# Optimization experiments

Hardware: AMD Instinct MI355X
Metric: run time of the kernel (lower is better)

## Reference

```python
import jax, jax.numpy as jnp
import numpy as np

B = 65536   # batch
F = 256     # FeatureDim
E = 8       # experts_num
D = 64      # ExpertOutDim
EPS = 1e-5  # BatchNorm eps (eval mode: running stats)


def _bn(x, g, be, m, v):
    # BatchNorm1d in eval mode
    return (x - m) * jax.lax.rsqrt(v + EPS) * g + be


def setup_inputs() -> dict:
    key = jax.random.key(0)
    ks = jax.random.split(key, 40)
    r = lambda i, s: jax.random.normal(ks[i], s, dtype=jnp.float32) * 0.05
    u = lambda i, s: jax.random.uniform(ks[i], s, dtype=jnp.float32)
    return dict(
        signal_em=jax.random.normal(ks[0], (B, F), dtype=jnp.float32),
        muti_em=jax.random.normal(ks[1], (B, F), dtype=jnp.float32),
        similarity=jax.random.uniform(ks[2], (B,), dtype=jnp.float32),
        w=u(3, ()), b=u(4, ()),
        ps_W=r(5, (F, 256)), ps_b=r(6, (256,)), ps_g=u(7, (256,)), ps_be=r(8, (256,)), ps_m=r(9, (256,)), ps_v=u(10, (256,)) + 0.5,
        pm_W=r(11, (F, 256)), pm_b=r(12, (256,)), pm_g=u(13, (256,)), pm_be=r(14, (256,)), pm_m=r(15, (256,)), pm_v=u(16, (256,)) + 0.5,
        c1_W=r(17, (2 * F, 64)), c1_b=r(18, (64,)), c1_g=u(19, (64,)), c1_be=r(20, (64,)), c1_m=r(21, (64,)), c1_v=u(22, (64,)) + 0.5,
        c2_W=r(23, (64, 64)), c2_b=r(24, (64,)), c2_g=u(25, (64,)), c2_be=r(26, (64,)), c2_m=r(27, (64,)), c2_v=u(28, (64,)) + 0.5,
        c3_W=r(29, (64, 2)), c3_b=r(30, (2,)),
        e_W1=r(31, (E, 2 * F, 256)), e_b1=r(32, (E, 256)),
        e_W2=r(33, (E, 256, D)), e_b2=r(34, (E, D)),
        s_W1=r(35, (E, E)), s_b1=r(36, (E,)), s_W2=r(37, (E, E)), s_b2=r(38, (E,)),
    )


def reference(signal_em, muti_em, similarity, w, b,
              ps_W, ps_b, ps_g, ps_be, ps_m, ps_v,
              pm_W, pm_b, pm_g, pm_be, pm_m, pm_v,
              c1_W, c1_b, c1_g, c1_be, c1_m, c1_v,
              c2_W, c2_b, c2_g, c2_be, c2_m, c2_v,
              c3_W, c3_b,
              e_W1, e_b1, e_W2, e_b2,
              s_W1, s_b1, s_W2, s_b2):
    sim_weight = similarity[:, None] * w + b                        # [B,1]
    sig = jax.nn.relu(_bn(signal_em @ ps_W + ps_b, ps_g, ps_be, ps_m, ps_v))
    sig = sim_weight * sig
    mut = jax.nn.relu(_bn(muti_em @ pm_W + pm_b, pm_g, pm_be, pm_m, pm_v))
    temp = jnp.concatenate([sig, mut], axis=1)                      # [B, 512]

    # classifier head (dropout = identity in eval mode)
    h = jax.nn.relu(_bn(temp @ c1_W + c1_b, c1_g, c1_be, c1_m, c1_v))
    h = jax.nn.relu(_bn(h @ c2_W + c2_b, c2_g, c2_be, c2_m, c2_v))
    pre_score = h @ c3_W + c3_b                                     # [B,2]

    # all E experts as one batched GEMM (Expert_net has dropout p=0)
    eh = jax.nn.relu(jnp.einsum('bf,efh->beh', temp, e_W1) + e_b1)  # [B,E,256]
    eo = jax.nn.relu(jnp.einsum('beh,ehd->bed', eh, e_W2) + e_b2)   # [B,E,64]

    # SE-style gating: avg/max pool over expert-out dim (kernel==D -> scalar)
    att_ave = eo.mean(axis=-1)                                      # [B,E]
    att_max = eo.max(axis=-1)                                       # [B,E]
    senet = lambda x: jax.nn.gelu(x @ s_W1 + s_b1, approximate=False) @ s_W2 + s_b2
    wts = jax.nn.sigmoid(senet(att_ave) + senet(att_max))           # [B,E]

    gate_out = jnp.einsum('bed,be->bd', eo, wts)                    # [B,D]
    return (gate_out, pre_score)
```

## Files before the change

kernel.cpp:

```cpp
#include <hip/hip_runtime.h>
#include <math.h>

using u32 = unsigned int;
using u16 = unsigned short;
typedef __attribute__((ext_vector_type(4))) float f4;
typedef __attribute__((ext_vector_type(4))) u32 u4;
typedef __attribute__((ext_vector_type(2))) u32 u2;
typedef __attribute__((ext_vector_type(8))) __bf16 b8;

union U4B8 { u4 u; b8 b; };

__device__ __forceinline__ u16 f2b(float x) {
  u32 u = __float_as_uint(x);
  u32 r = (u + 0x7FFFu + ((u >> 16) & 1u)) >> 16;
  return (u16)r;
}
__device__ __forceinline__ u32 pack2(float a, float b) { return (u32)f2b(a) | ((u32)f2b(b) << 16); }
__device__ __forceinline__ f4 mfma16(b8 a, b8 b, f4 c) {
  return __builtin_amdgcn_mfma_f32_16x16x32_bf16(a, b, c, 0, 0, 0);
}

#define FENCE() asm volatile("" ::: "memory")
#define RAWBAR() do { FENCE(); __builtin_amdgcn_s_barrier(); FENCE(); __builtin_amdgcn_sched_barrier(0); } while (0)
#define VMW(nlit) do { asm volatile("s_waitcnt vmcnt(" nlit ")" ::: "memory"); __builtin_amdgcn_sched_barrier(0); } while (0)
#define LGKM0() do { asm volatile("s_waitcnt lgkmcnt(0)" ::: "memory"); __builtin_amdgcn_sched_barrier(0); } while (0)
#define LBAR() do { LGKM0(); __builtin_amdgcn_s_barrier(); FENCE(); __builtin_amdgcn_sched_barrier(0); } while (0)

template <int NB>
__device__ __forceinline__ void gstage(const u16* g, u16* l, int t) {
#pragma unroll
  for (int i = 0; i < NB; i += 8192) {
    __builtin_amdgcn_global_load_lds(
        (__attribute__((address_space(1))) u32*)(g + (i >> 1) + t * 8),
        (__attribute__((address_space(3))) u32*)(l + (i >> 1) + ((t >> 6) << 9)),
        16, 0, 0);
  }
}

__global__ void prep_kernel(
    const float* __restrict__ ps_W, const float* __restrict__ ps_b, const float* __restrict__ ps_g,
    const float* __restrict__ ps_be, const float* __restrict__ ps_m, const float* __restrict__ ps_v,
    const float* __restrict__ pm_W, const float* __restrict__ pm_b, const float* __restrict__ pm_g,
    const float* __restrict__ pm_be, const float* __restrict__ pm_m, const float* __restrict__ pm_v,
    const float* __restrict__ c1_W, const float* __restrict__ c1_b, const float* __restrict__ c1_g,
    const float* __restrict__ c1_be, const float* __restrict__ c1_m, const float* __restrict__ c1_v,
    const float* __restrict__ c2_W, const float* __restrict__ c2_b, const float* __restrict__ c2_g,
    const float* __restrict__ c2_be, const float* __restrict__ c2_m, const float* __restrict__ c2_v,
    u16* __restrict__ pst, u16* __restrict__ pmt,
    u16* __restrict__ c1t, u16* __restrict__ c2t, float* __restrict__ fold)
{
  int i0 = blockIdx.x * blockDim.x + threadIdx.x;
  int stride = gridDim.x * blockDim.x;
  for (int idx = i0; idx < 65536; idx += stride) {
    int s = idx >> 14; int rem = idx & 16383;
    int n = rem >> 6, q = rem & 63;
    int k = s * 64 + (q ^ ((n & 7) << 3));
    pst[idx] = f2b(ps_W[k * 256 + n]);
    pmt[idx] = f2b(pm_W[k * 256 + n]);
  }
  for (int idx = i0; idx < 64 * 512; idx += stride) {
    int n = idx >> 9, q = idx & 511;
    int k = q ^ ((n & 7) << 3);
    c1t[idx] = f2b(c1_W[k * 64 + n]);
  }
  for (int idx = i0; idx < 64 * 64; idx += stride) {
    int n = idx >> 6, k = idx & 63;
    c2t[idx] = f2b(c2_W[k * 64 + n]);
  }
  for (int idx = i0; idx < 256; idx += stride) {
    float a = ps_g[idx] * rsqrtf(ps_v[idx] + 1e-5f);
    fold[idx] = a; fold[256 + idx] = (ps_b[idx] - ps_m[idx]) * a + ps_be[idx];
    float a2 = pm_g[idx] * rsqrtf(pm_v[idx] + 1e-5f);
    fold[512 + idx] = a2; fold[768 + idx] = (pm_b[idx] - pm_m[idx]) * a2 + pm_be[idx];
  }
  for (int idx = i0; idx < 64; idx += stride) {
    float a = c1_g[idx] * rsqrtf(c1_v[idx] + 1e-5f);
    fold[1024 + idx] = a; fold[1088 + idx] = (c1_b[idx] - c1_m[idx]) * a + c1_be[idx];
    float a2 = c2_g[idx] * rsqrtf(c2_v[idx] + 1e-5f);
    fold[1152 + idx] = a2; fold[1216 + idx] = (c2_b[idx] - c2_m[idx]) * a2 + c2_be[idx];
  }
}

__global__ __launch_bounds__(512, 4) void k1_kernel(
    const float* __restrict__ sig, const float* __restrict__ mut,
    const float* __restrict__ simil, const float* __restrict__ wS, const float* __restrict__ bS,
    const u16* __restrict__ pst, const u16* __restrict__ pmt,
    const float* __restrict__ fold, u16* __restrict__ temp,
    const float* __restrict__ e_W1, const float* __restrict__ e_W2,
    u16* __restrict__ w1t, u16* __restrict__ w2t)
{
  extern __shared__ __align__(16) u16 smk[];
  const int t = threadIdx.x;
  if (blockIdx.y == 2) {
    int i0 = blockIdx.x * 512 + t;
    const int stride = 1024 * 512;
    for (int idx = i0; idx < 8 * 256 * 512; idx += stride) {
      int e = idx >> 17; int rem = idx & 131071;
      int s = rem >> 14; int rem2 = rem & 16383;
      int n = rem2 >> 6; int q = rem2 & 63;
      int k = s * 64 + (q ^ ((n & 7) << 3));
      w1t[idx] = f2b(e_W1[e * 131072 + k * 256 + n]);
    }
    for (int idx = i0; idx < 8 * 64 * 256; idx += stride) {
      int e = idx >> 14; int rem = idx & 16383;
      int d = rem >> 8; int q = rem & 255;
      int h = q ^ ((d & 7) << 3);
      w2t[idx] = f2b(e_W2[e * 16384 + h * 64 + d]);
    }
    return;
  }
  const int w = t >> 6, l = t & 63;
  const int lr = l & 15, lk = (l >> 4) * 8, lv = (l >> 4) * 4;
  const int xoru = (l & 7) << 3;
  const int rg = w >> 1, cg = w & 1;
  const int half = blockIdx.y;
  const float* X = half ? mut : sig;
  const u16* Wt = half ? pmt : pst;
  const int rb = blockIdx.x;
  const int rg0 = rb * 64;
  const f4 ZF = {0.f, 0.f, 0.f, 0.f};
  const int myrow = rg * 16 + lr;

  f4 xr[16];
  {
    const float* xp = X + (rg0 + myrow) * 256 + lk;
#pragma unroll
    for (int c = 0; c < 8; ++c) {
      xr[2 * c]     = *(const f4*)(xp + c * 32);
      xr[2 * c + 1] = *(const f4*)(xp + c * 32 + 4);
    }
  }
  float swv = 1.f;
  if (half == 0) swv = simil[rg0 + myrow] * wS[0] + bS[0];
  gstage<32768>(Wt, smk, t);
  b8 af[8];
#pragma unroll
  for (int c = 0; c < 8; ++c) {
    U4B8 tmp;
    tmp.u[0] = pack2(xr[2 * c][0], xr[2 * c][1]);
    tmp.u[1] = pack2(xr[2 * c][2], xr[2 * c][3]);
    tmp.u[2] = pack2(xr[2 * c + 1][0], xr[2 * c + 1][1]);
    tmp.u[3] = pack2(xr[2 * c + 1][2], xr[2 * c + 1][3]);
    af[c] = tmp.b;
  }

  f4 acc[8];
#pragma unroll
  for (int i = 0; i < 8; ++i) acc[i] = ZF;

#define K1P(P, STG) do { \
    VMW("0"); RAWBAR(); \
    STG; \
    __builtin_amdgcn_s_setprio(1); \
    _Pragma("unroll") for (int kk = 0; kk < 2; ++kk) { \
      b8 bf[8]; \
      _Pragma("unroll") for (int nf = 0; nf < 8; ++nf) \
        bf[nf] = *(const b8*)(smk + ((P) & 1) * 16384 + (cg * 128 + nf * 16 + lr) * 64 + ((kk * 32 + lk) ^ xoru)); \
      _Pragma("unroll") for (int nf = 0; nf < 8; ++nf) \
        acc[nf] = mfma16(bf[nf], af[(P) * 2 + kk], acc[nf]); \
    } \
    __builtin_amdgcn_s_setprio(0); \
  } while (0)

  K1P(0, gstage<32768>(Wt + 16384, smk + 16384, t));
  K1P(1, gstage<32768>(Wt + 32768, smk, t));
  K1P(2, gstage<32768>(Wt + 49152, smk + 16384, t));
  K1P(3, (void)0);
#undef K1P

#pragma unroll
  for (int nf = 0; nf < 8; ++nf) {
    int col = cg * 128 + nf * 16 + lv;
    const f4 al = *(const f4*)(fold + half * 512 + col);
    const f4 be = *(const f4*)(fold + half * 512 + 256 + col);
    float v0 = fmaxf(acc[nf][0] * al[0] + be[0], 0.f) * swv;
    float v1 = fmaxf(acc[nf][1] * al[1] + be[1], 0.f) * swv;
    float v2 = fmaxf(acc[nf][2] * al[2] + be[2], 0.f) * swv;
    float v3 = fmaxf(acc[nf][3] * al[3] + be[3], 0.f) * swv;
    u2 pv; pv[0] = pack2(v0, v1); pv[1] = pack2(v2, v3);
    int st = col >> 6;
    int kin = col & 63;
    int q = kin ^ ((myrow & 7) << 3);
    *(u2*)(smk + st * 4096 + myrow * 64 + q) = pv;
  }
  LBAR();
  {
    u16* dst = temp + (rb >> 1) * 65536 + half * 32768 + (rb & 1) * 4096;
#pragma unroll
    for (int st = 0; st < 4; ++st) {
      u4 v = *(const u4*)(smk + st * 4096 + t * 8);
      *(u4*)(dst + st * 8192 + t * 8) = v;
    }
  }
}

__global__ __launch_bounds__(512, 2) void k2_kernel(
    u16* __restrict__ temp, const u16* __restrict__ w1t, const u16* __restrict__ w2t,
    const u16* __restrict__ c1t, const u16* __restrict__ c2t,
    const float* __restrict__ fold,
    const float* __restrict__ c3W, const float* __restrict__ c3B,
    const float* __restrict__ eb1, const float* __restrict__ eb2,
    const float* __restrict__ sW1, const float* __restrict__ sB1,
    const float* __restrict__ sW2, const float* __restrict__ sB2,
    float* __restrict__ outp)
{
  extern __shared__ __align__(16) u16 sm[];
  u16* smW  = sm;
  u16* smE  = sm + 32768;
  u16* smR2 = sm + 49152;
  float* attA  = (float*)(sm + 65536);
  float* attM  = attA + 1024;
  float* wtsb  = attM + 1024;
  float* c3sm  = wtsb + 1024;
  float* eb1sm = c3sm + 136;
  float* eb2sm = eb1sm + 2048;

  const int t = threadIdx.x, w = t >> 6, l = t & 63;
  const int lr = l & 15, lk = (l >> 4) * 8, lv = (l >> 4) * 4;
  const int xoru = (l & 7) << 3;
  const int rg = w >> 1, cg = w & 1;
  const int rg0 = blockIdx.x * 128;
  const f4 ZF = {0.f, 0.f, 0.f, 0.f};
  u16* tempE = temp + blockIdx.x * 65536;

  b8 af[16][2];

#define AFLOAD(R) { \
    _Pragma("unroll") for (int c8 = 0; c8 < 8; ++c8) { \
      _Pragma("unroll") for (int mi = 0; mi < 2; ++mi) \
        af[(R) * 8 + c8][mi] = *(const b8*)(smE + (c8 >> 1) * 8192 + (rg * 32 + mi * 16 + lr) * 64 + ((((c8 & 1) * 32) + lk) ^ xoru)); \
    } }

  {
    for (int z = t; z < 2048; z += 512) attA[z] = 0.f;
    f4 rEb1 = *(const f4*)(eb1 + t * 4);
    f4 rEb2 = ZF; if (t < 128) rEb2 = *(const f4*)(eb2 + t * 4);
    float rC3 = 0.f; if (t < 128) rC3 = c3W[t]; else if (t < 130) rC3 = c3B[t - 128];
    u4 rC2 = *(const u4*)(c2t + (t >> 3) * 64 + (t & 7) * 8);

    gstage<65536>(tempE, smE, t);
    gstage<65536>(c1t, smW, t);
    *(f4*)(eb1sm + t * 4) = rEb1;
    if (t < 128) *(f4*)(eb2sm + t * 4) = rEb2;
    if (t < 130) c3sm[t] = rC3;
    VMW("8"); RAWBAR();
    AFLOAD(0);
    asm volatile("s_waitcnt lgkmcnt(0)" ::: "memory");
    RAWBAR();
    gstage<65536>(tempE + 32768, smE, t);
    VMW("8"); RAWBAR();
    f4 ah[2][2] = {{ZF, ZF}, {ZF, ZF}};
#define HPART(R) { \
    __builtin_amdgcn_s_setprio(1); \
    _Pragma("unroll") for (int c8 = 0; c8 < 8; ++c8) { \
      _Pragma("unroll") for (int nf = 0; nf < 2; ++nf) { \
        b8 ch = *(const b8*)(smW + (cg * 32 + nf * 16 + lr) * 512 + ((((R) * 8 + c8) * 32 + lk) ^ xoru)); \
        _Pragma("unroll") for (int mi = 0; mi < 2; ++mi) \
          ah[nf][mi] = mfma16(ch, af[(R) * 8 + c8][mi], ah[nf][mi]); \
      } } \
    __builtin_amdgcn_s_setprio(0); }
    HPART(0)
    VMW("0"); RAWBAR();
    AFLOAD(1);
    HPART(1)
#undef HPART
    asm volatile("s_waitcnt lgkmcnt(0)" ::: "memory");
    RAWBAR();
    u16* h1b = smE;
    u16* c2sm = smR2;
    u16* h2b = smR2 + 4608;
#pragma unroll
    for (int nf = 0; nf < 2; ++nf) {
      int col = cg * 32 + nf * 16 + lv;
      const f4 av1 = *(const f4*)(fold + 1024 + col);
      const f4 bv1 = *(const f4*)(fold + 1088 + col);
#pragma unroll
      for (int mi = 0; mi < 2; ++mi) {
        int row = rg * 32 + mi * 16 + lr;
        u2 pv;
        pv[0] = pack2(fmaxf(ah[nf][mi][0] * av1[0] + bv1[0], 0.f), fmaxf(ah[nf][mi][1] * av1[1] + bv1[1], 0.f));
        pv[1] = pack2(fmaxf(ah[nf][mi][2] * av1[2] + bv1[2], 0.f), fmaxf(ah[nf][mi][3] * av1[3] + bv1[3], 0.f));
        *(u2*)(h1b + row * 72 + col) = pv;
      }
    }
    *(u4*)(c2sm + (t >> 3) * 72 + (t & 7) * 8) = rC2;
    LBAR();
    f4 a2[2][2] = {{ZF, ZF}, {ZF, ZF}};
#pragma unroll
    for (int kk = 0; kk < 2; ++kk) {
      b8 hf[2], cf[2];
#pragma unroll
      for (int mi = 0; mi < 2; ++mi)
        hf[mi] = *(const b8*)(h1b + (rg * 32 + mi * 16 + lr) * 72 + kk * 32 + lk);
#pragma unroll
      for (int nf = 0; nf < 2; ++nf)
        cf[nf] = *(const b8*)(c2sm + (cg * 32 + nf * 16 + lr) * 72 + kk * 32 + lk);
#pragma unroll
      for (int mi = 0; mi < 2; ++mi)
#pragma unroll
        for (int nf = 0; nf < 2; ++nf)
          a2[mi][nf] = mfma16(cf[nf], hf[mi], a2[mi][nf]);
    }
#pragma unroll
    for (int nf = 0; nf < 2; ++nf) {
      int col = cg * 32 + nf * 16 + lv;
      const f4 av2 = *(const f4*)(fold + 1152 + col);
      const f4 bv2 = *(const f4*)(fold + 1216 + col);
#pragma unroll
      for (int mi = 0; mi < 2; ++mi) {
        int row = rg * 32 + mi * 16 + lr;
        u2 pv;
        pv[0] = pack2(fmaxf(a2[mi][nf][0] * av2[0] + bv2[0], 0.f), fmaxf(a2[mi][nf][1] * av2[1] + bv2[1], 0.f));
        pv[1] = pack2(fmaxf(a2[mi][nf][2] * av2[2] + bv2[2], 0.f), fmaxf(a2[mi][nf][3] * av2[3] + bv2[3], 0.f));
        *(u2*)(h2b + row * 72 + col) = pv;
      }
    }
    LBAR();
    if (t < 256) {
      int row = t >> 1, c = t & 1;
      float s_ = c3sm[128 + c];
#pragma unroll
      for (int j = 0; j < 8; ++j) {
        u4 hv = *(const u4*)(h2b + row * 72 + j * 8);
#pragma unroll
        for (int q = 0; q < 4; ++q) {
          float lo = __uint_as_float(hv[q] << 16);
          float hi = __uint_as_float(hv[q] & 0xffff0000u);
          s_ += lo * c3sm[(j * 8 + q * 2) * 2 + c];
          s_ += hi * c3sm[(j * 8 + q * 2 + 1) * 2 + c];
        }
      }
      outp[4194304 + (rg0 + row) * 2 + c] = s_;
    }
    RAWBAR();
    gstage<32768>(w1t, smW, t);
  }

#define MPH(P, NW, ...) do { \
    VMW(NW); RAWBAR(); \
    __VA_ARGS__; \
    __builtin_amdgcn_s_setprio(1); \
    _Pragma("unroll") for (int kk = 0; kk < 2; ++kk) { \
      b8 bfA[4], bfB[4]; \
      _Pragma("unroll") for (int nf = 0; nf < 4; ++nf) \
        bfA[nf] = *(const b8*)(smW + ((P) & 1) * 16384 + (cg * 64 + nf * 16 + lr) * 64 + ((kk * 32 + lk) ^ xoru)); \
      _Pragma("unroll") for (int nf = 0; nf < 4; ++nf) \
        bfB[nf] = *(const b8*)(smW + ((P) & 1) * 16384 + 8192 + (cg * 64 + nf * 16 + lr) * 64 + ((kk * 32 + lk) ^ xoru)); \
      _Pragma("unroll") for (int nf = 0; nf < 4; ++nf) \
        _Pragma("unroll") for (int mi = 0; mi < 2; ++mi) \
          acc[nf][mi] = mfma16(bfA[nf], af[(P) * 2 + kk][mi], acc[nf][mi]); \
      _Pragma("unroll") for (int nf = 0; nf < 4; ++nf) \
        _Pragma("unroll") for (int mi = 0; mi < 2; ++mi) \
          acc[4 + nf][mi] = mfma16(bfB[nf], af[(P) * 2 + kk][mi], acc[4 + nf][mi]); \
    } \
    __builtin_amdgcn_s_setprio(0); \
  } while (0)

#define EHEPI(E, H, DST) { \
    _Pragma("unroll") for (int nf = 0; nf < 4; ++nf) { \
      int colL = cg * 64 + nf * 16 + lv; \
      const f4 bv = *(const f4*)(eb1sm + (E) * 256 + (H) * 128 + colL); \
      _Pragma("unroll") for (int mi = 0; mi < 2; ++mi) { \
        int row = rg * 32 + mi * 16 + lr; \
        f4 a_ = acc[(H) * 4 + nf][mi]; \
        u2 pv; \
        pv[0] = pack2(fmaxf(a_[0] + bv[0], 0.f), fmaxf(a_[1] + bv[1], 0.f)); \
        pv[1] = pack2(fmaxf(a_[2] + bv[2], 0.f), fmaxf(a_[3] + bv[3], 0.f)); \
        *(u2*)((DST) + row * 128 + (colL ^ xoru)) = pv; \
      } } }

#define G2ALL() do { \
    __builtin_amdgcn_s_setprio(1); \
    _Pragma("unroll") for (int kq = 0; kq < 8; ++kq) { \
      const u16* ebase = (kq < 4) ? smE : (smW + 16384); \
      b8 wf[2], ef[2]; \
      _Pragma("unroll") for (int nf = 0; nf < 2; ++nf) \
        wf[nf] = *(const b8*)(smR2 + (cg * 32 + nf * 16 + lr) * 256 + ((kq * 32 + lk) ^ xoru)); \
      _Pragma("unroll") for (int mi = 0; mi < 2; ++mi) \
        ef[mi] = *(const b8*)(ebase + (rg * 32 + mi * 16 + lr) * 128 + ((((kq & 3) * 32) + lk) ^ xoru)); \
      _Pragma("unroll") for (int mi = 0; mi < 2; ++mi) \
        _Pragma("unroll") for (int nf = 0; nf < 2; ++nf) \
          e2[mi][nf] = mfma16(wf[nf], ef[mi], e2[mi][nf]); \
    } \
    __builtin_amdgcn_s_setprio(0); \
  } while (0)

#define EXPERT(E, NWP0, NWG2) { \
    const u16* w1E = w1t + (E) * 131072; \
    f4 acc[8][2]; \
    _Pragma("unroll") for (int nf = 0; nf < 8; ++nf) \
      _Pragma("unroll") for (int mi = 0; mi < 2; ++mi) acc[nf][mi] = ZF; \
    MPH(0, NWP0, gstage<32768>(w1E + 1 * 16384, smW + 16384, t)); \
    MPH(1, "0",  gstage<32768>(w1E + 2 * 16384, smW, t)); \
    MPH(2, "0",  gstage<32768>(w1E + 3 * 16384, smW + 16384, t)); \
    MPH(3, "0",  gstage<32768>(w1E + 4 * 16384, smW, t)); \
    MPH(4, "0",  gstage<32768>(w1E + 5 * 16384, smW + 16384, t)); \
    MPH(5, "0",  gstage<32768>(w1E + 6 * 16384, smW, t)); \
    MPH(6, "0",  { gstage<32768>(w1E + 7 * 16384, smW + 16384, t); \
                   gstage<32768>(w2t + (E) * 16384, smR2, t); }); \
    MPH(7, "4",  { if ((E) < 7) gstage<32768>(w1t + ((E) + 1) * 131072, smW, t); }); \
    EHEPI(E, 0, smE) \
    RAWBAR();  \
    EHEPI(E, 1, smW + 16384) \
    VMW(NWG2); LBAR();  \
    f4 e2[2][2]; \
    e2[0][0] = ZF; e2[0][1] = ZF; e2[1][0] = ZF; e2[1][1] = ZF; \
    G2ALL(); \
     \
    _Pragma("unroll") for (int mi = 0; mi < 2; ++mi) { \
      int row = rg * 32 + mi * 16 + lr; \
      float s_ = 0.f, mx = 0.f; \
      _Pragma("unroll") for (int nf = 0; nf < 2; ++nf) { \
        int d0 = cg * 32 + nf * 16 + lv; \
        const f4 bv2 = *(const f4*)(eb2sm + (E) * 64 + d0); \
        float v0 = fmaxf(e2[mi][nf][0] + bv2[0], 0.f); \
        float v1 = fmaxf(e2[mi][nf][1] + bv2[1], 0.f); \
        float v2 = fmaxf(e2[mi][nf][2] + bv2[2], 0.f); \
        float v3 = fmaxf(e2[mi][nf][3] + bv2[3], 0.f); \
        s_ += v0 + v1 + v2 + v3; \
        mx = fmaxf(mx, fmaxf(fmaxf(v0, v1), fmaxf(v2, v3))); \
        u2 pv; pv[0] = pack2(v0, v1); pv[1] = pack2(v2, v3); \
        *(u2*)(tempE + (E) * 8192 + row * 64 + d0) = pv; \
      } \
      s_ += __shfl_xor(s_, 16); s_ += __shfl_xor(s_, 32); \
      mx = fmaxf(mx, __shfl_xor(mx, 16)); mx = fmaxf(mx, __shfl_xor(mx, 32)); \
      if (l < 16) { \
        atomicAdd(attA + row * 8 + (E), s_); \
        atomicMax((unsigned int*)(attM + row * 8 + (E)), __float_as_uint(mx)); \
      } \
    } \
  }

  EXPERT(0, "0", "4")
  EXPERT(1, "4", "4")
  EXPERT(2, "4", "4")
  EXPERT(3, "4", "4")
  EXPERT(4, "4", "4")
  EXPERT(5, "4", "4")
  EXPERT(6, "4", "4")
  EXPERT(7, "4", "0")
#undef EXPERT
#undef MPH
#undef EHEPI
#undef G2ALL

  VMW("0");
  LBAR();
  if (t < 128) {
    float xa[8], xm[8], ga[8], gm[8];
#pragma unroll
    for (int j = 0; j < 8; ++j) {
      xa[j] = attA[t * 8 + j] * 0.015625f;
      xm[j] = attM[t * 8 + j];
    }
#pragma unroll
    for (int j = 0; j < 8; ++j) {
      float a1 = sB1[j], a2 = sB1[j];
#pragma unroll
      for (int i = 0; i < 8; ++i) { float wv = sW1[i * 8 + j]; a1 += xa[i] * wv; a2 += xm[i] * wv; }
      ga[j] = 0.5f * a1 * (1.f + erff(a1 * 0.70710678118654752f));
      gm[j] = 0.5f * a2 * (1.f + erff(a2 * 0.70710678118654752f));
    }
#pragma unroll
    for (int j = 0; j < 8; ++j) {
      float o1 = sB2[j], o2 = sB2[j];
#pragma unroll
      for (int i = 0; i < 8; ++i) { float wv = sW2[i * 8 + j]; o1 += ga[i] * wv; o2 += gm[i] * wv; }
      float z = o1 + o2;
      wtsb[t * 8 + j] = 1.f / (1.f + expf(-z));
    }
  }
  LBAR();
  {
    int grow = t >> 2, gd0 = (t & 3) * 16;
    float wv[8];
#pragma unroll
    for (int e2_ = 0; e2_ < 8; ++e2_) wv[e2_] = wtsb[grow * 8 + e2_];
    float g[16];
#pragma unroll
    for (int j = 0; j < 16; ++j) g[j] = 0.f;
#pragma unroll
    for (int e2_ = 0; e2_ < 8; ++e2_) {
      const u16* wsE = tempE + e2_ * 8192 + grow * 64 + gd0;
      u4 qa = *(const u4*)(wsE); u4 qb = *(const u4*)(wsE + 8);
#pragma unroll
      for (int q = 0; q < 4; ++q) {
        g[2 * q + 0] += wv[e2_] * __uint_as_float(qa[q] << 16);
        g[2 * q + 1] += wv[e2_] * __uint_as_float(qa[q] & 0xffff0000u);
        g[8 + 2 * q + 0] += wv[e2_] * __uint_as_float(qb[q] << 16);
        g[8 + 2 * q + 1] += wv[e2_] * __uint_as_float(qb[q] & 0xffff0000u);
      }
    }
    float* op = outp + (rg0 + grow) * 64 + gd0;
    f4 o0 = {g[0], g[1], g[2], g[3]}, o1 = {g[4], g[5], g[6], g[7]};
    f4 o2 = {g[8], g[9], g[10], g[11]}, o3 = {g[12], g[13], g[14], g[15]};
    *(f4*)op = o0; *(f4*)(op + 4) = o1; *(f4*)(op + 8) = o2; *(f4*)(op + 12) = o3;
  }
}

extern "C" void kernel_launch(void* const* d_in, const int* in_sizes, int n_in,
                              void* d_out, int out_size, void* d_ws, size_t ws_size,
                              hipStream_t stream) {
  const float* signal = (const float*)d_in[0];
  const float* muti   = (const float*)d_in[1];
  const float* simil  = (const float*)d_in[2];
  const float* wS     = (const float*)d_in[3];
  const float* bS     = (const float*)d_in[4];
  const float* ps_W = (const float*)d_in[5];  const float* ps_b = (const float*)d_in[6];
  const float* ps_g = (const float*)d_in[7];  const float* ps_be = (const float*)d_in[8];
  const float* ps_m = (const float*)d_in[9];  const float* ps_v = (const float*)d_in[10];
  const float* pm_W = (const float*)d_in[11]; const float* pm_b = (const float*)d_in[12];
  const float* pm_g = (const float*)d_in[13]; const float* pm_be = (const float*)d_in[14];
  const float* pm_m = (const float*)d_in[15]; const float* pm_v = (const float*)d_in[16];
  const float* c1_W = (const float*)d_in[17]; const float* c1_b = (const float*)d_in[18];
  const float* c1_g = (const float*)d_in[19]; const float* c1_be = (const float*)d_in[20];
  const float* c1_m = (const float*)d_in[21]; const float* c1_v = (const float*)d_in[22];
  const float* c2_W = (const float*)d_in[23]; const float* c2_b = (const float*)d_in[24];
  const float* c2_g = (const float*)d_in[25]; const float* c2_be = (const float*)d_in[26];
  const float* c2_m = (const float*)d_in[27]; const float* c2_v = (const float*)d_in[28];
  const float* c3_W = (const float*)d_in[29]; const float* c3_b = (const float*)d_in[30];
  const float* e_W1 = (const float*)d_in[31]; const float* e_b1 = (const float*)d_in[32];
  const float* e_W2 = (const float*)d_in[33]; const float* e_b2 = (const float*)d_in[34];
  const float* s_W1 = (const float*)d_in[35]; const float* s_b1 = (const float*)d_in[36];
  const float* s_W2 = (const float*)d_in[37]; const float* s_b2 = (const float*)d_in[38];

  char* ws = (char*)d_ws;
  u16* temp = (u16*)ws;
  u16* w1t  = (u16*)(ws + 67108864);
  u16* w2t  = (u16*)(ws + 69206016);
  u16* pst  = (u16*)(ws + 69468160);
  u16* pmt  = (u16*)(ws + 69599232);
  u16* c1t  = (u16*)(ws + 69730304);
  u16* c2t  = (u16*)(ws + 69795840);
  float* fold = (float*)(ws + 69804032);
  float* outp = (float*)d_out;

  prep_kernel<<<dim3(256), dim3(256), 0, stream>>>(
      ps_W, ps_b, ps_g, ps_be, ps_m, ps_v, pm_W, pm_b, pm_g, pm_be, pm_m, pm_v,
      c1_W, c1_b, c1_g, c1_be, c1_m, c1_v, c2_W, c2_b, c2_g, c2_be, c2_m, c2_v,
      pst, pmt, c1t, c2t, fold);
  k1_kernel<<<dim3(1024, 3), dim3(512), 65536, stream>>>(
      signal, muti, simil, wS, bS, pst, pmt, fold, temp, e_W1, e_W2, w1t, w2t);
  k2_kernel<<<dim3(512), dim3(512), 154144, stream>>>(
      temp, w1t, w2t, c1t, c2t, fold, c3_W, c3_b, e_b1, e_b2, s_W1, s_b1, s_W2, s_b2, outp);
}
```

Before: 261.7 us.

## Load half of expert W1 fragments directly from global into registers

Splits each expert's first-layer weights into two halves. Columns 0-127 are still staged through shared memory. Columns 128-255 are pre-laid out in MFMA fragment order so each lane can load them straight from global memory into registers. This halves the LDS staging buffer for W1, which frees shared memory so the expert hidden upper half (ehHi) gets its own region and one barrier goes away. The c1 weight layout changes to match. In exchange the kernel issues more global loads per wave, carries more registers, and depends on finer vmcnt wait tuning.

```diff
diff --git a/kernel.cpp b/kernel.cpp
--- a/kernel.cpp
+++ b/kernel.cpp
@@ -59,8 +59,9 @@
     pmt[idx] = f2b(pm_W[k * 256 + n]);
   }
   for (int idx = i0; idx < 64 * 512; idx += stride) {
-    int n = idx >> 9, q = idx & 511;
-    int k = q ^ ((n & 7) << 3);
+    int R = idx >> 14; int rem = idx & 16383;
+    int n = rem >> 8, q = rem & 255;
+    int k = R * 256 + (q ^ ((n & 7) << 3));
     c1t[idx] = f2b(c1_W[k * 64 + n]);
   }
   for (int idx = i0; idx < 64 * 64; idx += stride) {
@@ -87,19 +88,29 @@
     const u16* __restrict__ pst, const u16* __restrict__ pmt,
     const float* __restrict__ fold, u16* __restrict__ temp,
     const float* __restrict__ e_W1, const float* __restrict__ e_W2,
-    u16* __restrict__ w1t, u16* __restrict__ w2t)
+    u16* __restrict__ w1t, u16* __restrict__ w1d, u16* __restrict__ w2t)
 {
   extern __shared__ __align__(16) u16 smk[];
   const int t = threadIdx.x;
   if (blockIdx.y == 2) {
     int i0 = blockIdx.x * 512 + t;
     const int stride = 1024 * 512;
-    for (int idx = i0; idx < 8 * 256 * 512; idx += stride) {
-      int e = idx >> 17; int rem = idx & 131071;
-      int s = rem >> 14; int rem2 = rem & 16383;
+    for (int idx = i0; idx < 8 * 8 * 128 * 64; idx += stride) {
+      int e = idx >> 16; int rem = idx & 65535;
+      int s = rem >> 13; int rem2 = rem & 8191;
       int n = rem2 >> 6; int q = rem2 & 63;
       int k = s * 64 + (q ^ ((n & 7) << 3));
       w1t[idx] = f2b(e_W1[e * 131072 + k * 256 + n]);
+    }
+    for (int idx = i0; idx < 8 * 8 * 16 * 512; idx += stride) {
+      int e = idx >> 16; int rem = idx & 65535;
+      int s = rem >> 13; int rem2 = rem & 8191;
+      int blk = rem2 >> 9; int li = rem2 & 511;
+      int cgi = blk >> 3, nfi = (blk >> 1) & 3, kki = blk & 1;
+      int l = li >> 3, j = li & 7;
+      int n = 128 + cgi * 64 + nfi * 16 + (l & 15);
+      int k = s * 64 + kki * 32 + (l >> 4) * 8 + j;
+      w1d[idx] = f2b(e_W1[e * 131072 + k * 256 + n]);
     }
     for (int idx = i0; idx < 8 * 64 * 256; idx += stride) {
       int e = idx >> 14; int rem = idx & 16383;
@@ -195,7 +206,8 @@
 }
 
 __global__ __launch_bounds__(512, 2) void k2_kernel(
-    u16* __restrict__ temp, const u16* __restrict__ w1t, const u16* __restrict__ w2t,
+    u16* __restrict__ temp, const u16* __restrict__ w1t, const u16* __restrict__ w1d,
+    const u16* __restrict__ w2t,
     const u16* __restrict__ c1t, const u16* __restrict__ c2t,
     const float* __restrict__ fold,
     const float* __restrict__ c3W, const float* __restrict__ c3B,
@@ -206,8 +218,9 @@
 {
   extern __shared__ __align__(16) u16 sm[];
   u16* smW  = sm;
-  u16* smE  = sm + 32768;
-  u16* smR2 = sm + 49152;
+  u16* smE  = sm + 16384;
+  u16* smR2 = sm + 32768;
+  u16* ehHi = sm + 49152;
   float* attA  = (float*)(sm + 65536);
   float* attM  = attA + 1024;
   float* wtsb  = attM + 1024;
@@ -239,7 +252,8 @@
     u4 rC2 = *(const u4*)(c2t + (t >> 3) * 64 + (t & 7) * 8);
 
     gstage<65536>(tempE, smE, t);
-    gstage<65536>(c1t, smW, t);
+    gstage<32768>(c1t, smW, t);
+    gstage<32768>(c1t + 16384, ehHi, t);
     *(f4*)(eb1sm + t * 4) = rEb1;
     if (t < 128) *(f4*)(eb2sm + t * 4) = rEb2;
     if (t < 130) c3sm[t] = rC3;
@@ -254,7 +268,7 @@
     __builtin_amdgcn_s_setprio(1); \
     _Pragma("unroll") for (int c8 = 0; c8 < 8; ++c8) { \
       _Pragma("unroll") for (int nf = 0; nf < 2; ++nf) { \
-        b8 ch = *(const b8*)(smW + (cg * 32 + nf * 16 + lr) * 512 + ((((R) * 8 + c8) * 32 + lk) ^ xoru)); \
+        b8 ch = *(const b8*)(((R) ? ehHi : smW) + (cg * 32 + nf * 16 + lr) * 256 + ((c8 * 32 + lk) ^ xoru)); \
         _Pragma("unroll") for (int mi = 0; mi < 2; ++mi) \
           ah[nf][mi] = mfma16(ch, af[(R) * 8 + c8][mi], ah[nf][mi]); \
       } } \
@@ -333,26 +347,32 @@
       outp[4194304 + (rg0 + row) * 2 + c] = s_;
     }
     RAWBAR();
-    gstage<32768>(w1t, smW, t);
-  }
-
-#define MPH(P, NW, ...) do { \
-    VMW(NW); RAWBAR(); \
+    gstage<16384>(w1t, smW, t);
+  }
+
+#define MPH(P, NWA, NWB, ...) do { \
+    b8 gB[8]; \
+    { const u16* bp = w1dE + (P) * 8192 + cg * 4096 + l * 8; \
+      _Pragma("unroll") for (int q = 0; q < 8; ++q) \
+        gB[q] = *(const b8*)(bp + q * 512); } \
+    VMW(NWA); RAWBAR(); \
     __VA_ARGS__; \
     __builtin_amdgcn_s_setprio(1); \
     _Pragma("unroll") for (int kk = 0; kk < 2; ++kk) { \
-      b8 bfA[4], bfB[4]; \
+      b8 bfA[4]; \
       _Pragma("unroll") for (int nf = 0; nf < 4; ++nf) \
-        bfA[nf] = *(const b8*)(smW + ((P) & 1) * 16384 + (cg * 64 + nf * 16 + lr) * 64 + ((kk * 32 + lk) ^ xoru)); \
-      _Pragma("unroll") for (int nf = 0; nf < 4; ++nf) \
-        bfB[nf] = *(const b8*)(smW + ((P) & 1) * 16384 + 8192 + (cg * 64 + nf * 16 + lr) * 64 + ((kk * 32 + lk) ^ xoru)); \
+        bfA[nf] = *(const b8*)(smW + ((P) & 1) * 8192 + (cg * 64 + nf * 16 + lr) * 64 + ((kk * 32 + lk) ^ xoru)); \
       _Pragma("unroll") for (int nf = 0; nf < 4; ++nf) \
         _Pragma("unroll") for (int mi = 0; mi < 2; ++mi) \
           acc[nf][mi] = mfma16(bfA[nf], af[(P) * 2 + kk][mi], acc[nf][mi]); \
+    } \
+    __builtin_amdgcn_s_setprio(0); \
+    VMW(NWB); \
+    __builtin_amdgcn_s_setprio(1); \
+    _Pragma("unroll") for (int kk = 0; kk < 2; ++kk) \
       _Pragma("unroll") for (int nf = 0; nf < 4; ++nf) \
         _Pragma("unroll") for (int mi = 0; mi < 2; ++mi) \
-          acc[4 + nf][mi] = mfma16(bfB[nf], af[(P) * 2 + kk][mi], acc[4 + nf][mi]); \
-    } \
+          acc[4 + nf][mi] = mfma16(gB[nf * 2 + kk], af[(P) * 2 + kk][mi], acc[4 + nf][mi]); \
     __builtin_amdgcn_s_setprio(0); \
   } while (0)
 
@@ -372,7 +392,7 @@
 #define G2ALL() do { \
     __builtin_amdgcn_s_setprio(1); \
     _Pragma("unroll") for (int kq = 0; kq < 8; ++kq) { \
-      const u16* ebase = (kq < 4) ? smE : (smW + 16384); \
+      const u16* ebase = (kq < 4) ? smE : ehHi; \
       b8 wf[2], ef[2]; \
       _Pragma("unroll") for (int nf = 0; nf < 2; ++nf) \
         wf[nf] = *(const b8*)(smR2 + (cg * 32 + nf * 16 + lr) * 256 + ((kq * 32 + lk) ^ xoru)); \
@@ -385,24 +405,24 @@
     __builtin_amdgcn_s_setprio(0); \
   } while (0)
 
-#define EXPERT(E, NWP0, NWG2) { \
-    const u16* w1E = w1t + (E) * 131072; \
+#define EXPERT(E, NWA0, NWB7) { \
+    const u16* w1E = w1t + (E) * 65536; \
+    const u16* w1dE = w1d + (E) * 65536; \
     f4 acc[8][2]; \
     _Pragma("unroll") for (int nf = 0; nf < 8; ++nf) \
       _Pragma("unroll") for (int mi = 0; mi < 2; ++mi) acc[nf][mi] = ZF; \
-    MPH(0, NWP0, gstage<32768>(w1E + 1 * 16384, smW + 16384, t)); \
-    MPH(1, "0",  gstage<32768>(w1E + 2 * 16384, smW, t)); \
-    MPH(2, "0",  gstage<32768>(w1E + 3 * 16384, smW + 16384, t)); \
-    MPH(3, "0",  gstage<32768>(w1E + 4 * 16384, smW, t)); \
-    MPH(4, "0",  gstage<32768>(w1E + 5 * 16384, smW + 16384, t)); \
-    MPH(5, "0",  gstage<32768>(w1E + 6 * 16384, smW, t)); \
-    MPH(6, "0",  { gstage<32768>(w1E + 7 * 16384, smW + 16384, t); \
-                   gstage<32768>(w2t + (E) * 16384, smR2, t); }); \
-    MPH(7, "4",  { if ((E) < 7) gstage<32768>(w1t + ((E) + 1) * 131072, smW, t); }); \
+    MPH(0, NWA0, "2", gstage<16384>(w1E + 1 * 8192, smW + 8192, t)); \
+    MPH(1, "8", "2",  gstage<16384>(w1E + 2 * 8192, smW, t)); \
+    MPH(2, "8", "2",  gstage<16384>(w1E + 3 * 8192, smW + 8192, t)); \
+    MPH(3, "8", "2",  gstage<16384>(w1E + 4 * 8192, smW, t)); \
+    MPH(4, "8", "2",  gstage<16384>(w1E + 5 * 8192, smW + 8192, t)); \
+    MPH(5, "8", "2",  gstage<16384>(w1E + 6 * 8192, smW, t)); \
+    MPH(6, "8", "6",  { gstage<16384>(w1E + 7 * 8192, smW + 8192, t); \
+                        gstage<32768>(w2t + (E) * 16384, smR2, t); }); \
+    MPH(7, "12", NWB7, { if ((E) < 7) gstage<16384>(w1t + ((E) + 1) * 65536, smW, t); }); \
     EHEPI(E, 0, smE) \
-    RAWBAR();  \
-    EHEPI(E, 1, smW + 16384) \
-    VMW(NWG2); LBAR();  \
+    EHEPI(E, 1, ehHi) \
+    LBAR();  \
     f4 e2[2][2]; \
     e2[0][0] = ZF; e2[0][1] = ZF; e2[1][0] = ZF; e2[1][1] = ZF; \
     G2ALL(); \
@@ -431,14 +451,14 @@
     } \
   }
 
-  EXPERT(0, "0", "4")
-  EXPERT(1, "4", "4")
-  EXPERT(2, "4", "4")
-  EXPERT(3, "4", "4")
-  EXPERT(4, "4", "4")
-  EXPERT(5, "4", "4")
-  EXPERT(6, "4", "4")
-  EXPERT(7, "4", "0")
+  EXPERT(0, "8",  "2")
+  EXPERT(1, "12", "2")
+  EXPERT(2, "12", "2")
+  EXPERT(3, "12", "2")
+  EXPERT(4, "12", "2")
+  EXPERT(5, "12", "2")
+  EXPERT(6, "12", "2")
+  EXPERT(7, "12", "0")
 #undef EXPERT
 #undef MPH
 #undef EHEPI
@@ -527,6 +547,7 @@
   char* ws = (char*)d_ws;
   u16* temp = (u16*)ws;
   u16* w1t  = (u16*)(ws + 67108864);
+  u16* w1d  = (u16*)(ws + 68157440);
   u16* w2t  = (u16*)(ws + 69206016);
   u16* pst  = (u16*)(ws + 69468160);
   u16* pmt  = (u16*)(ws + 69599232);
@@ -540,7 +561,7 @@
       c1_W, c1_b, c1_g, c1_be, c1_m, c1_v, c2_W, c2_b, c2_g, c2_be, c2_m, c2_v,
       pst, pmt, c1t, c2t, fold);
   k1_kernel<<<dim3(1024, 3), dim3(512), 65536, stream>>>(
-      signal, muti, simil, wS, bS, pst, pmt, fold, temp, e_W1, e_W2, w1t, w2t);
+      signal, muti, simil, wS, bS, pst, pmt, fold, temp, e_W1, e_W2, w1t, w1d, w2t);
   k2_kernel<<<dim3(512), dim3(512), 154144, stream>>>(
-      temp, w1t, w2t, c1t, c2t, fold, c3_W, c3_b, e_b1, e_b2, s_W1, s_b1, s_W2, s_b2, outp);
-}
+      temp, w1t, w1d, w2t, c1t, c2t, fold, c3_W, c3_b, e_b1, e_b2, s_W1, s_b1, s_W2, s_b2, outp);
+}
```

Result: slower. 349.3 us (+33.5%).

## Defer second expert GEMM half and pooling into next expert's first-layer phases

Applied to the files above, without the earlier changes.

Splits the per-expert second-layer GEMM into two halves. Only the half reading the smW buffer runs immediately. The half reading smE (RIDQ) is interleaved into the first four MFMA phases of the next expert, and the pooling/atomics epilogue runs after phase 3. The aim is to hide the serialized second-layer compute and epilogue behind the next expert's weight loads and MFMA work, cutting pipeline bubbles between experts. The cost is higher register pressure from keeping e2 live across phases, plus changed wait counts (NW4 moved to phase 4) that must still keep smE and smR2 valid until they are consumed.

```diff
diff --git a/kernel.cpp b/kernel.cpp
--- a/kernel.cpp
+++ b/kernel.cpp
@@ -336,9 +336,12 @@
     gstage<32768>(w1t, smW, t);
   }
 
-#define MPH(P, NW, ...) do { \
+  f4 e2[2][2];
+  e2[0][0] = ZF; e2[0][1] = ZF; e2[1][0] = ZF; e2[1][1] = ZF;
+
+#define MPH(P, NW, STG, RID) do { \
     VMW(NW); RAWBAR(); \
-    __VA_ARGS__; \
+    STG; \
     __builtin_amdgcn_s_setprio(1); \
     _Pragma("unroll") for (int kk = 0; kk < 2; ++kk) { \
       b8 bfA[4], bfB[4]; \
@@ -353,7 +356,19 @@
         _Pragma("unroll") for (int mi = 0; mi < 2; ++mi) \
           acc[4 + nf][mi] = mfma16(bfB[nf], af[(P) * 2 + kk][mi], acc[4 + nf][mi]); \
     } \
+    RID; \
     __builtin_amdgcn_s_setprio(0); \
+  } while (0)
+
+#define RIDQ(KQ) do { \
+    b8 wf0 = *(const b8*)(smR2 + (cg * 32 + lr) * 256 + (((KQ) * 32 + lk) ^ xoru)); \
+    b8 wf1 = *(const b8*)(smR2 + (cg * 32 + 16 + lr) * 256 + (((KQ) * 32 + lk) ^ xoru)); \
+    b8 ef0 = *(const b8*)(smE + (rg * 32 + lr) * 128 + (((KQ) * 32 + lk) ^ xoru)); \
+    b8 ef1 = *(const b8*)(smE + (rg * 32 + 16 + lr) * 128 + (((KQ) * 32 + lk) ^ xoru)); \
+    e2[0][0] = mfma16(wf0, ef0, e2[0][0]); \
+    e2[0][1] = mfma16(wf1, ef0, e2[0][1]); \
+    e2[1][0] = mfma16(wf0, ef1, e2[1][0]); \
+    e2[1][1] = mfma16(wf1, ef1, e2[1][1]); \
   } while (0)
 
 #define EHEPI(E, H, DST) { \
@@ -369,15 +384,14 @@
         *(u2*)((DST) + row * 128 + (colL ^ xoru)) = pv; \
       } } }
 
-#define G2ALL() do { \
+#define G2HI() do { \
     __builtin_amdgcn_s_setprio(1); \
-    _Pragma("unroll") for (int kq = 0; kq < 8; ++kq) { \
-      const u16* ebase = (kq < 4) ? smE : (smW + 16384); \
+    _Pragma("unroll") for (int kq = 4; kq < 8; ++kq) { \
       b8 wf[2], ef[2]; \
       _Pragma("unroll") for (int nf = 0; nf < 2; ++nf) \
         wf[nf] = *(const b8*)(smR2 + (cg * 32 + nf * 16 + lr) * 256 + ((kq * 32 + lk) ^ xoru)); \
       _Pragma("unroll") for (int mi = 0; mi < 2; ++mi) \
-        ef[mi] = *(const b8*)(ebase + (rg * 32 + mi * 16 + lr) * 128 + ((((kq & 3) * 32) + lk) ^ xoru)); \
+        ef[mi] = *(const b8*)(smW + 16384 + (rg * 32 + mi * 16 + lr) * 128 + (((kq - 4) * 32 + lk) ^ xoru)); \
       _Pragma("unroll") for (int mi = 0; mi < 2; ++mi) \
         _Pragma("unroll") for (int nf = 0; nf < 2; ++nf) \
           e2[mi][nf] = mfma16(wf[nf], ef[mi], e2[mi][nf]); \
@@ -385,34 +399,13 @@
     __builtin_amdgcn_s_setprio(0); \
   } while (0)
 
-#define EXPERT(E, NWP0, NWG2) { \
-    const u16* w1E = w1t + (E) * 131072; \
-    f4 acc[8][2]; \
-    _Pragma("unroll") for (int nf = 0; nf < 8; ++nf) \
-      _Pragma("unroll") for (int mi = 0; mi < 2; ++mi) acc[nf][mi] = ZF; \
-    MPH(0, NWP0, gstage<32768>(w1E + 1 * 16384, smW + 16384, t)); \
-    MPH(1, "0",  gstage<32768>(w1E + 2 * 16384, smW, t)); \
-    MPH(2, "0",  gstage<32768>(w1E + 3 * 16384, smW + 16384, t)); \
-    MPH(3, "0",  gstage<32768>(w1E + 4 * 16384, smW, t)); \
-    MPH(4, "0",  gstage<32768>(w1E + 5 * 16384, smW + 16384, t)); \
-    MPH(5, "0",  gstage<32768>(w1E + 6 * 16384, smW, t)); \
-    MPH(6, "0",  { gstage<32768>(w1E + 7 * 16384, smW + 16384, t); \
-                   gstage<32768>(w2t + (E) * 16384, smR2, t); }); \
-    MPH(7, "4",  { if ((E) < 7) gstage<32768>(w1t + ((E) + 1) * 131072, smW, t); }); \
-    EHEPI(E, 0, smE) \
-    RAWBAR();  \
-    EHEPI(E, 1, smW + 16384) \
-    VMW(NWG2); LBAR();  \
-    f4 e2[2][2]; \
-    e2[0][0] = ZF; e2[0][1] = ZF; e2[1][0] = ZF; e2[1][1] = ZF; \
-    G2ALL(); \
-     \
+#define POOLX(EE) do { \
     _Pragma("unroll") for (int mi = 0; mi < 2; ++mi) { \
       int row = rg * 32 + mi * 16 + lr; \
       float s_ = 0.f, mx = 0.f; \
       _Pragma("unroll") for (int nf = 0; nf < 2; ++nf) { \
         int d0 = cg * 32 + nf * 16 + lv; \
-        const f4 bv2 = *(const f4*)(eb2sm + (E) * 64 + d0); \
+        const f4 bv2 = *(const f4*)(eb2sm + (EE) * 64 + d0); \
         float v0 = fmaxf(e2[mi][nf][0] + bv2[0], 0.f); \
         float v1 = fmaxf(e2[mi][nf][1] + bv2[1], 0.f); \
         float v2 = fmaxf(e2[mi][nf][2] + bv2[2], 0.f); \
@@ -420,29 +413,57 @@
         s_ += v0 + v1 + v2 + v3; \
         mx = fmaxf(mx, fmaxf(fmaxf(v0, v1), fmaxf(v2, v3))); \
         u2 pv; pv[0] = pack2(v0, v1); pv[1] = pack2(v2, v3); \
-        *(u2*)(tempE + (E) * 8192 + row * 64 + d0) = pv; \
+        *(u2*)(tempE + (EE) * 8192 + row * 64 + d0) = pv; \
       } \
       s_ += __shfl_xor(s_, 16); s_ += __shfl_xor(s_, 32); \
       mx = fmaxf(mx, __shfl_xor(mx, 16)); mx = fmaxf(mx, __shfl_xor(mx, 32)); \
       if (l < 16) { \
-        atomicAdd(attA + row * 8 + (E), s_); \
-        atomicMax((unsigned int*)(attM + row * 8 + (E)), __float_as_uint(mx)); \
+        atomicAdd(attA + row * 8 + (EE), s_); \
+        atomicMax((unsigned int*)(attM + row * 8 + (EE)), __float_as_uint(mx)); \
       } \
     } \
-  }
-
-  EXPERT(0, "0", "4")
-  EXPERT(1, "4", "4")
-  EXPERT(2, "4", "4")
-  EXPERT(3, "4", "4")
-  EXPERT(4, "4", "4")
-  EXPERT(5, "4", "4")
-  EXPERT(6, "4", "4")
-  EXPERT(7, "4", "0")
+  } while (0)
+
+#define EXPERT(E, NW4, NWG2S, R0, R1_, R2_, R3_, PST) { \
+    const u16* w1E = w1t + (E) * 131072; \
+    f4 acc[8][2]; \
+    _Pragma("unroll") for (int nf = 0; nf < 8; ++nf) \
+      _Pragma("unroll") for (int mi = 0; mi < 2; ++mi) acc[nf][mi] = ZF; \
+    MPH(0, "0", gstage<32768>(w1E + 1 * 16384, smW + 16384, t), R0); \
+    MPH(1, "0", gstage<32768>(w1E + 2 * 16384, smW, t), R1_); \
+    MPH(2, "0", gstage<32768>(w1E + 3 * 16384, smW + 16384, t), R2_); \
+    MPH(3, "0", gstage<32768>(w1E + 4 * 16384, smW, t), R3_); \
+    PST; \
+    MPH(4, NW4, gstage<32768>(w1E + 5 * 16384, smW + 16384, t), (void)0); \
+    MPH(5, "0", gstage<32768>(w1E + 6 * 16384, smW, t), (void)0); \
+    MPH(6, "0", { gstage<32768>(w1E + 7 * 16384, smW + 16384, t); \
+                  gstage<32768>(w2t + (E) * 16384, smR2, t); }, (void)0); \
+    MPH(7, "4", { if ((E) < 7) gstage<32768>(w1t + ((E) + 1) * 131072, smW, t); }, (void)0); \
+    EHEPI(E, 0, smE) \
+    RAWBAR();  \
+    EHEPI(E, 1, smW + 16384) \
+    VMW(NWG2S); LBAR();  \
+    e2[0][0] = ZF; e2[0][1] = ZF; e2[1][0] = ZF; e2[1][1] = ZF; \
+    G2HI(); \
+  }
+
+  EXPERT(0, "0", "4", (void)0, (void)0, (void)0, (void)0, (void)0)
+  EXPERT(1, "4", "4", RIDQ(0), RIDQ(1), RIDQ(2), RIDQ(3), POOLX(0))
+  EXPERT(2, "4", "4", RIDQ(0), RIDQ(1), RIDQ(2), RIDQ(3), POOLX(1))
+  EXPERT(3, "4", "4", RIDQ(0), RIDQ(1), RIDQ(2), RIDQ(3), POOLX(2))
+  EXPERT(4, "4", "4", RIDQ(0), RIDQ(1), RIDQ(2), RIDQ(3), POOLX(3))
+  EXPERT(5, "4", "4", RIDQ(0), RIDQ(1), RIDQ(2), RIDQ(3), POOLX(4))
+  EXPERT(6, "4", "4", RIDQ(0), RIDQ(1), RIDQ(2), RIDQ(3), POOLX(5))
+  EXPERT(7, "4", "0", RIDQ(0), RIDQ(1), RIDQ(2), RIDQ(3), POOLX(6))
+  __builtin_amdgcn_s_setprio(1);
+  RIDQ(0); RIDQ(1); RIDQ(2); RIDQ(3);
+  __builtin_amdgcn_s_setprio(0);
+  POOLX(7);
 #undef EXPERT
 #undef MPH
+#undef RIDQ
 #undef EHEPI
-#undef G2ALL
+#undef G2HI
 
   VMW("0");
   LBAR();
```

Result: slower. 286.4 us (+9.4%).

## Split expert W1 staging into quarter-size buffers for deeper prefetch pipeline

Applied to the files above, without the earlier changes.

Reorganizes the pre-transposed expert W1 layout into 16 sub-tiles of 8192 elements (each k-chunk split into two 128-column halves). The per-expert GEMM loop now cycles through four 16 KB LDS slots instead of two 32 KB slots. This keeps two loads in flight and lets each barrier wait on a smaller chunk. The aim is to hide global-load latency behind MFMA work, at the cost of twice as many barriers per expert and more fragile vmcnt bookkeeping.

```diff
diff --git a/kernel.cpp b/kernel.cpp
--- a/kernel.cpp
+++ b/kernel.cpp
@@ -96,9 +96,10 @@
     const int stride = 1024 * 512;
     for (int idx = i0; idx < 8 * 256 * 512; idx += stride) {
       int e = idx >> 17; int rem = idx & 131071;
-      int s = rem >> 14; int rem2 = rem & 16383;
-      int n = rem2 >> 6; int q = rem2 & 63;
-      int k = s * 64 + (q ^ ((n & 7) << 3));
+      int S = rem >> 13; int rem2 = rem & 8191;
+      int nl = rem2 >> 6; int q = rem2 & 63;
+      int n = (S & 1) * 128 + nl;
+      int k = (S >> 1) * 64 + (q ^ ((nl & 7) << 3));
       w1t[idx] = f2b(e_W1[e * 131072 + k * 256 + n]);
     }
     for (int idx = i0; idx < 8 * 64 * 256; idx += stride) {
@@ -336,25 +337,22 @@
     gstage<32768>(w1t, smW, t);
   }
 
-#define MPH(P, NW, ...) do { \
+#define SUB(S, NW, STG) do { \
     VMW(NW); RAWBAR(); \
-    __VA_ARGS__; \
+    STG; \
     __builtin_amdgcn_s_setprio(1); \
     _Pragma("unroll") for (int kk = 0; kk < 2; ++kk) { \
-      b8 bfA[4], bfB[4]; \
+      b8 bf[4]; \
       _Pragma("unroll") for (int nf = 0; nf < 4; ++nf) \
-        bfA[nf] = *(const b8*)(smW + ((P) & 1) * 16384 + (cg * 64 + nf * 16 + lr) * 64 + ((kk * 32 + lk) ^ xoru)); \
-      _Pragma("unroll") for (int nf = 0; nf < 4; ++nf) \
-        bfB[nf] = *(const b8*)(smW + ((P) & 1) * 16384 + 8192 + (cg * 64 + nf * 16 + lr) * 64 + ((kk * 32 + lk) ^ xoru)); \
+        bf[nf] = *(const b8*)(smW + ((S) & 3) * 8192 + (cg * 64 + nf * 16 + lr) * 64 + ((kk * 32 + lk) ^ xoru)); \
       _Pragma("unroll") for (int nf = 0; nf < 4; ++nf) \
         _Pragma("unroll") for (int mi = 0; mi < 2; ++mi) \
-          acc[nf][mi] = mfma16(bfA[nf], af[(P) * 2 + kk][mi], acc[nf][mi]); \
-      _Pragma("unroll") for (int nf = 0; nf < 4; ++nf) \
-        _Pragma("unroll") for (int mi = 0; mi < 2; ++mi) \
-          acc[4 + nf][mi] = mfma16(bfB[nf], af[(P) * 2 + kk][mi], acc[4 + nf][mi]); \
+          acc[((S) & 1) * 4 + nf][mi] = mfma16(bf[nf], af[((S) >> 1) * 2 + kk][mi], acc[((S) & 1) * 4 + nf][mi]); \
     } \
     __builtin_amdgcn_s_setprio(0); \
   } while (0)
+
+#define G16(SRC, DST) gstage<16384>((SRC), (DST), t)
 
 #define EHEPI(E, H, DST) { \
     _Pragma("unroll") for (int nf = 0; nf < 4; ++nf) { \
@@ -385,34 +383,13 @@
     __builtin_amdgcn_s_setprio(0); \
   } while (0)
 
-#define EXPERT(E, NWP0, NWG2) { \
-    const u16* w1E = w1t + (E) * 131072; \
-    f4 acc[8][2]; \
-    _Pragma("unroll") for (int nf = 0; nf < 8; ++nf) \
-      _Pragma("unroll") for (int mi = 0; mi < 2; ++mi) acc[nf][mi] = ZF; \
-    MPH(0, NWP0, gstage<32768>(w1E + 1 * 16384, smW + 16384, t)); \
-    MPH(1, "0",  gstage<32768>(w1E + 2 * 16384, smW, t)); \
-    MPH(2, "0",  gstage<32768>(w1E + 3 * 16384, smW + 16384, t)); \
-    MPH(3, "0",  gstage<32768>(w1E + 4 * 16384, smW, t)); \
-    MPH(4, "0",  gstage<32768>(w1E + 5 * 16384, smW + 16384, t)); \
-    MPH(5, "0",  gstage<32768>(w1E + 6 * 16384, smW, t)); \
-    MPH(6, "0",  { gstage<32768>(w1E + 7 * 16384, smW + 16384, t); \
-                   gstage<32768>(w2t + (E) * 16384, smR2, t); }); \
-    MPH(7, "4",  { if ((E) < 7) gstage<32768>(w1t + ((E) + 1) * 131072, smW, t); }); \
-    EHEPI(E, 0, smE) \
-    RAWBAR();  \
-    EHEPI(E, 1, smW + 16384) \
-    VMW(NWG2); LBAR();  \
-    f4 e2[2][2]; \
-    e2[0][0] = ZF; e2[0][1] = ZF; e2[1][0] = ZF; e2[1][1] = ZF; \
-    G2ALL(); \
-     \
+#define POOLX(EE) do { \
     _Pragma("unroll") for (int mi = 0; mi < 2; ++mi) { \
       int row = rg * 32 + mi * 16 + lr; \
       float s_ = 0.f, mx = 0.f; \
       _Pragma("unroll") for (int nf = 0; nf < 2; ++nf) { \
         int d0 = cg * 32 + nf * 16 + lv; \
-        const f4 bv2 = *(const f4*)(eb2sm + (E) * 64 + d0); \
+        const f4 bv2 = *(const f4*)(eb2sm + (EE) * 64 + d0); \
         float v0 = fmaxf(e2[mi][nf][0] + bv2[0], 0.f); \
         float v1 = fmaxf(e2[mi][nf][1] + bv2[1], 0.f); \
         float v2 = fmaxf(e2[mi][nf][2] + bv2[2], 0.f); \
@@ -420,27 +397,60 @@
         s_ += v0 + v1 + v2 + v3; \
         mx = fmaxf(mx, fmaxf(fmaxf(v0, v1), fmaxf(v2, v3))); \
         u2 pv; pv[0] = pack2(v0, v1); pv[1] = pack2(v2, v3); \
-        *(u2*)(tempE + (E) * 8192 + row * 64 + d0) = pv; \
+        *(u2*)(tempE + (EE) * 8192 + row * 64 + d0) = pv; \
       } \
       s_ += __shfl_xor(s_, 16); s_ += __shfl_xor(s_, 32); \
       mx = fmaxf(mx, __shfl_xor(mx, 16)); mx = fmaxf(mx, __shfl_xor(mx, 32)); \
       if (l < 16) { \
-        atomicAdd(attA + row * 8 + (E), s_); \
-        atomicMax((unsigned int*)(attM + row * 8 + (E)), __float_as_uint(mx)); \
+        atomicAdd(attA + row * 8 + (EE), s_); \
+        atomicMax((unsigned int*)(attM + row * 8 + (EE)), __float_as_uint(mx)); \
       } \
     } \
-  }
-
-  EXPERT(0, "0", "4")
-  EXPERT(1, "4", "4")
-  EXPERT(2, "4", "4")
-  EXPERT(3, "4", "4")
-  EXPERT(4, "4", "4")
-  EXPERT(5, "4", "4")
-  EXPERT(6, "4", "4")
-  EXPERT(7, "4", "0")
+  } while (0)
+
+#define EXPERT(E, NW0, NW1, NW15, NWPOST) { \
+    const u16* w1E = w1t + (E) * 131072; \
+    f4 acc[8][2]; \
+    _Pragma("unroll") for (int nf = 0; nf < 8; ++nf) \
+      _Pragma("unroll") for (int mi = 0; mi < 2; ++mi) acc[nf][mi] = ZF; \
+    SUB(0, NW0, G16(w1E + 2 * 8192, smW + 2 * 8192)); \
+    SUB(1, NW1, G16(w1E + 3 * 8192, smW + 3 * 8192)); \
+    SUB(2, "2", G16(w1E + 4 * 8192, smW + 0 * 8192)); \
+    SUB(3, "2", G16(w1E + 5 * 8192, smW + 1 * 8192)); \
+    SUB(4, "2", G16(w1E + 6 * 8192, smW + 2 * 8192)); \
+    SUB(5, "2", G16(w1E + 7 * 8192, smW + 3 * 8192)); \
+    SUB(6, "2", G16(w1E + 8 * 8192, smW + 0 * 8192)); \
+    SUB(7, "2", G16(w1E + 9 * 8192, smW + 1 * 8192)); \
+    SUB(8, "2", G16(w1E + 10 * 8192, smW + 2 * 8192)); \
+    SUB(9, "2", G16(w1E + 11 * 8192, smW + 3 * 8192)); \
+    SUB(10, "2", G16(w1E + 12 * 8192, smW + 0 * 8192)); \
+    SUB(11, "2", G16(w1E + 13 * 8192, smW + 1 * 8192)); \
+    SUB(12, "2", G16(w1E + 14 * 8192, smW + 2 * 8192)); \
+    SUB(13, "2", { G16(w1E + 15 * 8192, smW + 3 * 8192); \
+                   gstage<32768>(w2t + (E) * 16384, smR2, t); }); \
+    SUB(14, "6", { if ((E) < 7) G16(w1t + ((E) + 1) * 131072, smW); }); \
+    SUB(15, NW15, { if ((E) < 7) G16(w1t + ((E) + 1) * 131072 + 8192, smW + 8192); }); \
+    EHEPI(E, 0, smE) \
+    RAWBAR();  \
+    EHEPI(E, 1, smW + 16384) \
+    VMW(NWPOST); LBAR();  \
+    f4 e2[2][2]; \
+    e2[0][0] = ZF; e2[0][1] = ZF; e2[1][0] = ZF; e2[1][1] = ZF; \
+    G2ALL(); \
+    POOLX(E); \
+  }
+
+  EXPERT(0, "2", "2", "6", "4")
+  EXPERT(1, "6", "6", "6", "4")
+  EXPERT(2, "6", "6", "6", "4")
+  EXPERT(3, "6", "6", "6", "4")
+  EXPERT(4, "6", "6", "6", "4")
+  EXPERT(5, "6", "6", "6", "4")
+  EXPERT(6, "6", "6", "6", "4")
+  EXPERT(7, "6", "6", "4", "0")
 #undef EXPERT
-#undef MPH
+#undef SUB
+#undef G16
 #undef EHEPI
 #undef G2ALL
 
```

Result: no change. 262.0 us (+0.1%).
